# Kernel optimization log

Hardware: AMD Instinct MI355X
Metric: run time of the kernel (lower is better)

## Reference

```python
import jax, jax.numpy as jnp
import numpy as np

B, L, SH, EH, A, T = 128, 200, 512, 512, 512, 3


def setup_inputs() -> dict:
    key = jax.random.key(0)
    ks = jax.random.split(key, 13)
    s = 0.05  # small init scale to keep tanh/sigmoid unsaturated
    return {
        "sent_enc_doc": jax.random.normal(ks[0], (B, L, 2 * SH), jnp.float32),
        "h0_w": jax.random.normal(ks[1], (EH, SH), jnp.float32) * s,
        "h0_b": jax.random.normal(ks[2], (EH,), jnp.float32) * s,
        "gru_w_ih": jax.random.normal(ks[3], (3 * EH, 2 * SH), jnp.float32) * s,
        "gru_w_hh": jax.random.normal(ks[4], (3 * EH, EH), jnp.float32) * s,
        "gru_b_ih": jax.random.normal(ks[5], (3 * EH,), jnp.float32) * s,
        "gru_b_hh": jax.random.normal(ks[6], (3 * EH,), jnp.float32) * s,
        "wq": jax.random.normal(ks[7], (A, EH), jnp.float32) * s,
        "bq": jax.random.normal(ks[8], (A,), jnp.float32) * s,
        "wd": jax.random.normal(ks[9], (A, 2 * SH), jnp.float32) * s,
        "bd": jax.random.normal(ks[10], (A,), jnp.float32) * s,
        "ws": jax.random.normal(ks[11], (1, A), jnp.float32) * s,
        "bs": jax.random.normal(ks[12], (1,), jnp.float32) * s,
    }


def reference(sent_enc_doc, h0_w, h0_b, gru_w_ih, gru_w_hh, gru_b_ih, gru_b_hh,
              wq, bq, wd, bd, ws, bs):
    b, l, d2 = sent_enc_doc.shape
    sh = d2 // 2
    eh = gru_w_hh.shape[1]
    neg = jnp.asarray(-1e6, sent_enc_doc.dtype)

    # h0 = tanh(W * last backward vector), replicated across doc_len
    last_back = sent_enc_doc[:, 0, sh:]                      # (B, SH)
    h0 = jnp.tanh(last_back @ h0_w.T + h0_b)                 # (B, EH)
    h = jnp.broadcast_to(h0[:, None, :], (b, l, eh))         # (B, L, EH)

    s_prev = jnp.zeros((b, l, d2), sent_enc_doc.dtype)
    d_proj = sent_enc_doc @ wd.T + bd                        # (B, L, A) - loop-invariant
    mask = jnp.zeros((b, l), bool)
    rows = jnp.arange(b)

    scores_list, sel_list = [], []
    for _ in range(T):  # fixed, tiny, sequentially-dependent loop
        # GRUCell (torch gate order: r, z, n)
        gx = s_prev @ gru_w_ih.T + gru_b_ih                  # (B, L, 3EH)
        gh = h @ gru_w_hh.T + gru_b_hh                       # (B, L, 3EH)
        xr, xz, xn = jnp.split(gx, 3, axis=-1)
        hr, hz, hn = jnp.split(gh, 3, axis=-1)
        r = jax.nn.sigmoid(xr + hr)
        z = jax.nn.sigmoid(xz + hz)
        n = jnp.tanh(xn + r * hn)
        h = (1.0 - z) * n + z * h                            # (B, L, EH)

        # scorer: ws . tanh(Wq h + Wd s_i)
        score = (jnp.tanh(h @ wq.T + bq + d_proj) @ ws.T + bs)[..., 0]  # (B, L)
        score = jnp.where(mask, neg, score)
        idx = jnp.argmax(score, axis=1)                      # (B,)
        mask = mask.at[rows, idx].set(True)

        # gather the selected sentence encoding, broadcast to all positions
        s_sel = jnp.take_along_axis(sent_enc_doc, idx[:, None, None], axis=1)  # (B,1,2SH)
        s_prev = jnp.broadcast_to(s_sel, (b, l, d2))

        scores_list.append(score)
        sel_list.append(idx)

    sents_scores = jnp.stack(scores_list, axis=1)            # (B, T, L)
    sents_selected = jnp.stack(sel_list, axis=1)             # (B, T)
    return sents_scores, sents_selected
```

## Files before the change

### kernel.cpp

```cpp
#include <hip/hip_runtime.h>
#include <hip/hip_bf16.h>

constexpr int Bn  = 128;
constexpr int Ln  = 200;
constexpr int D2n = 1024;
constexpr int G3n = 1536;
constexpr int Tn  = 3;
constexpr int Nn  = 512;
constexpr int Kn  = 1024;

typedef unsigned short ushort;
typedef float f32x4 __attribute__((ext_vector_type(4)));
typedef __bf16 bf16x8 __attribute__((ext_vector_type(8)));

__device__ __forceinline__ ushort f2bf(float f) {
  unsigned u = __float_as_uint(f);
  unsigned r = (u + 0x7fffu + ((u >> 16) & 1u)) >> 16;
  return (ushort)r;
}
__device__ __forceinline__ float bf2f(ushort h) {
  return __uint_as_float(((unsigned)h) << 16);
}

__device__ __forceinline__ void gld_lds16(const ushort* g, ushort* l) {
  __builtin_amdgcn_global_load_lds(
      (const __attribute__((address_space(1))) unsigned int*)g,
      (__attribute__((address_space(3))) unsigned int*)l, 16, 0, 0);
}

__device__ __forceinline__ float ftanh(float x) {
  float cx = fminf(fmaxf(x, -15.f), 15.f);
  float e  = __expf(2.f * cx);
  return (e - 1.f) * __builtin_amdgcn_rcpf(e + 1.f);
}

__global__ void k_split(const float* __restrict__ W, ushort* __restrict__ hi,
                        ushort* __restrict__ lo) {
  int i = blockIdx.x * 256 + threadIdx.x;
  float4 v = ((const float4*)W)[i];
  ushort4 h, l;
  h.x = f2bf(v.x); l.x = f2bf(v.x - bf2f(h.x));
  h.y = f2bf(v.y); l.y = f2bf(v.y - bf2f(h.y));
  h.z = f2bf(v.z); l.z = f2bf(v.z - bf2f(h.z));
  h.w = f2bf(v.w); l.w = f2bf(v.w - bf2f(h.w));
  ((ushort4*)hi)[i] = h;
  ((ushort4*)lo)[i] = l;
}

__global__ void k_split3(const float* __restrict__ w_ih, const float* __restrict__ w_hh,
                         ushort* __restrict__ WihH, ushort* __restrict__ WihL,
                         ushort* __restrict__ WhhH, ushort* __restrict__ WhhL) {
  int i = blockIdx.x * 256 + threadIdx.x;
  const float* src; ushort* hi; ushort* lo; int off;
  if (i < 393216) { src = w_ih; hi = WihH; lo = WihL; off = i; }
  else            { src = w_hh; hi = WhhH; lo = WhhL; off = i - 393216; }
  float4 v = ((const float4*)src)[off];
  ushort4 h, l;
  h.x = f2bf(v.x); l.x = f2bf(v.x - bf2f(h.x));
  h.y = f2bf(v.y); l.y = f2bf(v.y - bf2f(h.y));
  h.z = f2bf(v.z); l.z = f2bf(v.z - bf2f(h.z));
  h.w = f2bf(v.w); l.w = f2bf(v.w - bf2f(h.w));
  ((ushort4*)hi)[off] = h;
  ((ushort4*)lo)[off] = l;
}

__global__ void k_transp(const float* __restrict__ in, float* __restrict__ out,
                         int R, int C) {
  __shared__ float t[32][33];
  const int x = threadIdx.x, y = threadIdx.y;
  const int c0 = blockIdx.x * 32, r0 = blockIdx.y * 32;
  #pragma unroll
  for (int i = 0; i < 4; ++i)
    t[y + i * 8][x] = in[(size_t)(r0 + y + i * 8) * C + c0 + x];
  __syncthreads();
  #pragma unroll
  for (int i = 0; i < 4; ++i)
    out[(size_t)(c0 + y + i * 8) * R + r0 + x] = t[x][y + i * 8];
}

__launch_bounds__(256)
__global__ void k_h0(const float* __restrict__ sent, const float* __restrict__ W,
                     const float* __restrict__ bias, float* __restrict__ out,
                     ushort* __restrict__ outh, ushort* __restrict__ outl) {
  __shared__ float s[16 * 512];
  const int b0 = blockIdx.y * 16;
  const int jl = threadIdx.x & 63;
  const int j  = blockIdx.x * 64 + jl;
  const int bg = (threadIdx.x >> 6) * 4;

  for (int i = threadIdx.x; i < 2048; i += 256) {
    int r = i >> 7, c = i & 127;
    ((float4*)s)[i] = *(const float4*)(sent + (size_t)(b0 + r) * (Ln * D2n) + 512 + c * 4);
  }
  __syncthreads();

  const float4* w4 = (const float4*)(W + (size_t)j * 512);
  const float4* r0 = (const float4*)(s + (size_t)(bg + 0) * 512);
  const float4* r1 = (const float4*)(s + (size_t)(bg + 1) * 512);
  const float4* r2 = (const float4*)(s + (size_t)(bg + 2) * 512);
  const float4* r3 = (const float4*)(s + (size_t)(bg + 3) * 512);

  float acc0 = 0.f, acc1 = 0.f, acc2 = 0.f, acc3 = 0.f;
  #pragma unroll 4
  for (int k4 = 0; k4 < 128; ++k4) {
    float4 wv = w4[k4];
    float4 a;
    a = r0[k4]; acc0 += wv.x*a.x + wv.y*a.y + wv.z*a.z + wv.w*a.w;
    a = r1[k4]; acc1 += wv.x*a.x + wv.y*a.y + wv.z*a.z + wv.w*a.w;
    a = r2[k4]; acc2 += wv.x*a.x + wv.y*a.y + wv.z*a.z + wv.w*a.w;
    a = r3[k4]; acc3 += wv.x*a.x + wv.y*a.y + wv.z*a.z + wv.w*a.w;
  }
  float bb = bias[j];
  float accs[4] = {acc0, acc1, acc2, acc3};
  #pragma unroll
  for (int i = 0; i < 4; ++i) {
    float v = tanhf(accs[i] + bb);
    size_t o = (size_t)(b0 + bg + i) * 512 + j;
    out[o] = v;
    ushort hv = f2bf(v);
    outh[o] = hv;
    outl[o] = f2bf(v - bf2f(hv));
  }
}

template<int KK>
__device__ __forceinline__ void mfma_tile128(
    const ushort* __restrict__ Ah, const ushort* __restrict__ Al,
    const ushort* __restrict__ Bh, const ushort* __restrict__ Bl,
    const float* __restrict__ bias, float* __restrict__ C, int ldc,
    int m0, int n0) {
  __shared__ __align__(16) ushort sAh[128 * 32];
  __shared__ __align__(16) ushort sAl[128 * 32];
  __shared__ __align__(16) ushort sBh[128 * 32];
  __shared__ __align__(16) ushort sBl[128 * 32];

  const int tid  = threadIdx.x;
  const int wave = tid >> 6, lane = tid & 63;
  const int wy = (wave >> 1) * 64, wx = (wave & 1) * 64;
  const int lm = lane & 15, lq = lane >> 4;
  const int fs = (lq ^ ((lm >> 1) & 3)) * 8;

  const int S0 = (wave * 2 + 0) * 64 + lane;
  const int S1 = (wave * 2 + 1) * 64 + lane;
  const int r0 = S0 >> 2, r1 = S1 >> 2;
  const int c0 = ((S0 & 3) ^ ((r0 >> 1) & 3)) * 8;
  const int c1 = ((S1 & 3) ^ ((r1 >> 1) & 3)) * 8;
  const ushort* pAh0 = Ah + (size_t)(m0 + r0) * KK + c0;
  const ushort* pAh1 = Ah + (size_t)(m0 + r1) * KK + c1;
  const ushort* pAl0 = Al + (size_t)(m0 + r0) * KK + c0;
  const ushort* pAl1 = Al + (size_t)(m0 + r1) * KK + c1;
  const ushort* pBh0 = Bh + (size_t)(n0 + r0) * KK + c0;
  const ushort* pBh1 = Bh + (size_t)(n0 + r1) * KK + c1;
  const ushort* pBl0 = Bl + (size_t)(n0 + r0) * KK + c0;
  const ushort* pBl1 = Bl + (size_t)(n0 + r1) * KK + c1;
  ushort* dA0 = &sAh[S0 * 8]; ushort* dA1 = &sAh[S1 * 8];
  ushort* dL0 = &sAl[S0 * 8]; ushort* dL1 = &sAl[S1 * 8];
  ushort* dB0 = &sBh[S0 * 8]; ushort* dB1 = &sBh[S1 * 8];
  ushort* dC0 = &sBl[S0 * 8]; ushort* dC1 = &sBl[S1 * 8];

  f32x4 acc[4][4] = {};

  for (int ks = 0; ks < KK / 32; ++ks) {
    const int ko = ks * 32;
    gld_lds16(pAh0 + ko, dA0); gld_lds16(pAh1 + ko, dA1);
    gld_lds16(pAl0 + ko, dL0); gld_lds16(pAl1 + ko, dL1);
    gld_lds16(pBh0 + ko, dB0); gld_lds16(pBh1 + ko, dB1);
    gld_lds16(pBl0 + ko, dC0); gld_lds16(pBl1 + ko, dC1);
    __syncthreads();

    bf16x8 ah[4], al[4], bh[4], bl[4];
    #pragma unroll
    for (int mi = 0; mi < 4; ++mi) {
      const int o = (wy + mi * 16 + lm) * 32 + fs;
      ah[mi] = *(const bf16x8*)&sAh[o];
      al[mi] = *(const bf16x8*)&sAl[o];
    }
    #pragma unroll
    for (int ni = 0; ni < 4; ++ni) {
      const int o = (wx + ni * 16 + lm) * 32 + fs;
      bh[ni] = *(const bf16x8*)&sBh[o];
      bl[ni] = *(const bf16x8*)&sBl[o];
    }
    #pragma unroll
    for (int mi = 0; mi < 4; ++mi)
      #pragma unroll
      for (int ni = 0; ni < 4; ++ni) {
        acc[mi][ni] = __builtin_amdgcn_mfma_f32_16x16x32_bf16(ah[mi], bh[ni], acc[mi][ni], 0, 0, 0);
        acc[mi][ni] = __builtin_amdgcn_mfma_f32_16x16x32_bf16(ah[mi], bl[ni], acc[mi][ni], 0, 0, 0);
        acc[mi][ni] = __builtin_amdgcn_mfma_f32_16x16x32_bf16(al[mi], bh[ni], acc[mi][ni], 0, 0, 0);
      }
    __syncthreads();
  }

  #pragma unroll
  for (int ni = 0; ni < 4; ++ni) {
    int col = n0 + wx + ni * 16 + lm;
    float bb = bias[col];
    #pragma unroll
    for (int mi = 0; mi < 4; ++mi) {
      int rbase = m0 + wy + mi * 16 + lq * 4;
      #pragma unroll
      for (int r = 0; r < 4; ++r)
        C[(size_t)(rbase + r) * ldc + col] = acc[mi][ni][r] + bb;
    }
  }
}

__launch_bounds__(256)
__global__ void k_dproj_mfma(const ushort* __restrict__ Ahi, const ushort* __restrict__ Alo,
                             const ushort* __restrict__ Whi, const ushort* __restrict__ Wlo,
                             const float* __restrict__ bias, float* __restrict__ C) {
  const int bid = blockIdx.x;
  mfma_tile128<1024>(Ahi, Alo, Whi, Wlo, bias, C, Nn, (bid % 200) * 128, (bid / 200) * 128);
}

__launch_bounds__(256)
__global__ void k_gates(const ushort* __restrict__ sxh, const ushort* __restrict__ sxl,
                        const float* __restrict__ hOld,
                        const ushort* __restrict__ hh, const ushort* __restrict__ hl,
                        const ushort* __restrict__ WihH, const ushort* __restrict__ WihL,
                        const ushort* __restrict__ WhhH, const ushort* __restrict__ WhhL,
                        const float* __restrict__ b_ih, const float* __restrict__ b_hh,
                        float* __restrict__ hNew, ushort* __restrict__ hhN,
                        ushort* __restrict__ hlN) {
  __shared__ __align__(16) ushort sAh[2][2][64 * 32];
  __shared__ __align__(16) ushort sAl[2][2][64 * 32];
  __shared__ __align__(16) ushort sWh[2][2][48 * 32];
  __shared__ __align__(16) ushort sWl[2][2][48 * 32];

  const int bb  = blockIdx.x >> 5;
  const int j0  = (blockIdx.x & 31) * 16;
  const int rb0 = bb * 64;
  const int tid = threadIdx.x, wave = tid >> 6, lane = tid & 63;
  const int wy = wave * 16;
  const int lm = lane & 15, lq = lane >> 4;
  const int fs = (lq ^ ((lm >> 1) & 3)) * 8;

  const int rA = tid >> 2;
  const int cA = ((tid & 3) ^ ((rA >> 1) & 3)) * 8;
  const bool wOn = tid < 192;
  const int gw = (rA >> 4) * 512 + j0 + (rA & 15);

  const ushort* sxh_r = sxh + (size_t)(rb0 + rA) * 1024 + cA;
  const ushort* sxl_r = sxl + (size_t)(rb0 + rA) * 1024 + cA;
  const ushort* hh_r  = hh  + (size_t)(rb0 + rA) * 512  + cA;
  const ushort* hl_r  = hl  + (size_t)(rb0 + rA) * 512  + cA;
  const ushort* wih_h = WihH + (size_t)gw * 1024 + cA;
  const ushort* wih_l = WihL + (size_t)gw * 1024 + cA;
  const ushort* whh_h = WhhH + (size_t)gw * 512 + cA;
  const ushort* whh_l = WhhL + (size_t)gw * 512 + cA;

  auto stage = [&](int s, int buf) {
    if (s < 16) {
      const int ko = s * 64;
      #pragma unroll
      for (int kk = 0; kk < 2; ++kk) {
        gld_lds16(sxh_r + ko + kk * 32, &sAh[buf][kk][tid * 8]);
        gld_lds16(sxl_r + ko + kk * 32, &sAl[buf][kk][tid * 8]);
        if (wOn) {
          gld_lds16(wih_h + ko + kk * 32, &sWh[buf][kk][tid * 8]);
          gld_lds16(wih_l + ko + kk * 32, &sWl[buf][kk][tid * 8]);
        }
      }
    } else {
      const int ko = (s - 16) * 64;
      #pragma unroll
      for (int kk = 0; kk < 2; ++kk) {
        gld_lds16(hh_r + ko + kk * 32, &sAh[buf][kk][tid * 8]);
        gld_lds16(hl_r + ko + kk * 32, &sAl[buf][kk][tid * 8]);
        if (wOn) {
          gld_lds16(whh_h + ko + kk * 32, &sWh[buf][kk][tid * 8]);
          gld_lds16(whh_l + ko + kk * 32, &sWl[buf][kk][tid * 8]);
        }
      }
    }
  };

  f32x4 ax[3] = {};
  f32x4 ag[3] = {};

  auto compute = [&](int cur, f32x4 (&acc)[3]) {
    const int oA = (wy + lm) * 32 + fs;
    #pragma unroll
    for (int kk = 0; kk < 2; ++kk) {
      bf16x8 fah = *(const bf16x8*)&sAh[cur][kk][oA];
      bf16x8 fal = *(const bf16x8*)&sAl[cur][kk][oA];
      #pragma unroll
      for (int g = 0; g < 3; ++g) {
        const int oW = (g * 16 + lm) * 32 + fs;
        bf16x8 fbh = *(const bf16x8*)&sWh[cur][kk][oW];
        bf16x8 fbl = *(const bf16x8*)&sWl[cur][kk][oW];
        acc[g] = __builtin_amdgcn_mfma_f32_16x16x32_bf16(fah, fbh, acc[g], 0, 0, 0);
        acc[g] = __builtin_amdgcn_mfma_f32_16x16x32_bf16(fah, fbl, acc[g], 0, 0, 0);
        acc[g] = __builtin_amdgcn_mfma_f32_16x16x32_bf16(fal, fbh, acc[g], 0, 0, 0);
      }
    }
  };

  stage(0, 0);
  asm volatile("s_waitcnt vmcnt(0)" ::: "memory");

  for (int s = 0; s < 24; ++s) {
    const int cur = s & 1, nxt = cur ^ 1;
    __syncthreads();
    if (s + 1 < 24) stage(s + 1, nxt);
    if (s < 16) compute(cur, ax); else compute(cur, ag);
    if (s + 1 < 24)
      asm volatile("s_waitcnt vmcnt(0)" ::: "memory");
  }

  const int j = j0 + lm;
  const float bir = b_ih[j], biz = b_ih[512 + j], bin = b_ih[1024 + j];
  const float bhr = b_hh[j], bhz = b_hh[512 + j], bhn = b_hh[1024 + j];
  #pragma unroll
  for (int rr = 0; rr < 4; ++rr) {
    const int b = rb0 + wy + lq * 4 + rr;
    float xr = ax[0][rr] + bir, hr = ag[0][rr] + bhr;
    float xz = ax[1][rr] + biz, hz = ag[1][rr] + bhz;
    float xn = ax[2][rr] + bin, hn = ag[2][rr] + bhn;
    float r = 1.f / (1.f + expf(-(xr + hr)));
    float z = 1.f / (1.f + expf(-(xz + hz)));
    float n = tanhf(xn + r * hn);
    float hv = hOld[(size_t)b * 512 + j];
    float hw = (1.f - z) * n + z * hv;
    hNew[(size_t)b * 512 + j] = hw;
    ushort hbf = f2bf(hw);
    hhN[(size_t)b * 512 + j] = hbf;
    hlN[(size_t)b * 512 + j] = f2bf(hw - bf2f(hbf));
  }
}

__launch_bounds__(256)
__global__ void k_score_argmax(const float* __restrict__ dproj, const float* __restrict__ h,
                               const float* __restrict__ wqT, const float* __restrict__ bq,
                               const float* __restrict__ wsv, const float* __restrict__ bsv,
                               const float* __restrict__ sent,
                               ushort* __restrict__ s_rowh, ushort* __restrict__ s_rowl,
                               int* __restrict__ mask, float* __restrict__ outScores,
                               float* __restrict__ outSel, int t) {
  const int b = blockIdx.x;
  const int tid = threadIdx.x, lane = tid & 63, wv = tid >> 6;
  __shared__ float shb[512];
  __shared__ float sq[512];
  __shared__ float ssc[Ln];
  __shared__ int s_idx;

  if (tid < 128)
    ((float4*)shb)[tid] = ((const float4*)(h + (size_t)b * 512))[tid];
  __syncthreads();

  float qx = 0.f, qy = 0.f;
  #pragma unroll 8
  for (int k = 0; k < 512; ++k) {
    float hk = shb[k];
    float2 w = ((const float2*)(wqT + (size_t)k * 512))[tid];
    qx += hk * w.x; qy += hk * w.y;
  }
  sq[tid * 2]     = qx + bq[tid * 2];
  sq[tid * 2 + 1] = qy + bq[tid * 2 + 1];
  __syncthreads();

  const float4* q4  = (const float4*)sq;
  const float4* ws4 = (const float4*)wsv;
  const float4 qq0 = q4[lane],  qq1 = q4[lane + 64];
  const float4 wv0 = ws4[lane], wv1 = ws4[lane + 64];
  const float bs0 = bsv[0];

  for (int l = wv; l < Ln; l += 4) {
    const float4* dp4 = (const float4*)(dproj + ((size_t)b * Ln + l) * Nn);
    float4 d0 = dp4[lane], d1 = dp4[lane + 64];
    float sum = ftanh(qq0.x + d0.x) * wv0.x + ftanh(qq0.y + d0.y) * wv0.y
              + ftanh(qq0.z + d0.z) * wv0.z + ftanh(qq0.w + d0.w) * wv0.w
              + ftanh(qq1.x + d1.x) * wv1.x + ftanh(qq1.y + d1.y) * wv1.y
              + ftanh(qq1.z + d1.z) * wv1.z + ftanh(qq1.w + d1.w) * wv1.w;
    #pragma unroll
    for (int off = 32; off > 0; off >>= 1) sum += __shfl_xor(sum, off, 64);
    if (lane == 0) {
      float v = sum + bs0;
      if (mask[b * Ln + l]) v = -1000000.0f;
      ssc[l] = v;
      outScores[(size_t)b * (Tn * Ln) + t * Ln + l] = v;
    }
  }
  __syncthreads();

  if (tid < 64) {
    float best = -3.0e38f; int bi = 0;
    for (int l = tid; l < Ln; l += 64) {
      float v = ssc[l];
      if (v > best) { best = v; bi = l; }
    }
    #pragma unroll
    for (int off = 32; off > 0; off >>= 1) {
      float ov = __shfl_down(best, off, 64);
      int   oi = __shfl_down(bi,   off, 64);
      if (ov > best || (ov == best && oi < bi)) { best = ov; bi = oi; }
    }
    if (tid == 0) s_idx = bi;
  }
  __syncthreads();
  int idx = s_idx;
  const float* src = sent + ((size_t)b * Ln + idx) * D2n;
  int k = tid * 4;
  float4 v = *(const float4*)(src + k);
  ushort4 hvec, lvec;
  hvec.x = f2bf(v.x); lvec.x = f2bf(v.x - bf2f(hvec.x));
  hvec.y = f2bf(v.y); lvec.y = f2bf(v.y - bf2f(hvec.y));
  hvec.z = f2bf(v.z); lvec.z = f2bf(v.z - bf2f(hvec.z));
  hvec.w = f2bf(v.w); lvec.w = f2bf(v.w - bf2f(hvec.w));
  *(ushort4*)(s_rowh + (size_t)b * 1024 + k) = hvec;
  *(ushort4*)(s_rowl + (size_t)b * 1024 + k) = lvec;
  if (tid == 0) {
    mask[b * Ln + idx] = 1;
    outSel[(size_t)b * Tn + t] = (float)idx;
  }
}

extern "C" void kernel_launch(void* const* d_in, const int* in_sizes, int n_in,
                              void* d_out, int out_size, void* d_ws, size_t ws_size,
                              hipStream_t stream) {
  const float* sent = (const float*)d_in[0];
  const float* h0_w = (const float*)d_in[1];
  const float* h0_b = (const float*)d_in[2];
  const float* w_ih = (const float*)d_in[3];
  const float* w_hh = (const float*)d_in[4];
  const float* b_ih = (const float*)d_in[5];
  const float* b_hh = (const float*)d_in[6];
  const float* wq   = (const float*)d_in[7];
  const float* bq   = (const float*)d_in[8];
  const float* wd   = (const float*)d_in[9];
  const float* bd   = (const float*)d_in[10];
  const float* wsv  = (const float*)d_in[11];
  const float* bsv  = (const float*)d_in[12];

  float* wsf     = (float*)d_ws;
  float* d_proj  = wsf;
  float* hA      = d_proj + 13107200;
  float* hB      = hA + 65536;
  int*   mask    = (int*)(hB + 65536);
  ushort* Whi    = (ushort*)(mask + 25600);
  ushort* Wlo    = Whi + 524288;
  ushort* hhA    = Wlo + 524288;
  ushort* hlA    = hhA + 65536;
  ushort* hhB    = hlA + 65536;
  ushort* hlB    = hhB + 65536;
  ushort* s_rowh = hlB + 65536;
  ushort* s_rowl = s_rowh + 131072;
  ushort* Ahi    = s_rowl + 131072;
  ushort* Alo    = Ahi + 26214400;

  ushort* WihH   = Ahi;
  ushort* WihL   = WihH + 1572864;
  ushort* WhhH   = WihL + 1572864;
  ushort* WhhL   = WhhH + 786432;
  float*  wqT    = (float*)(WhhL + 786432);

  float* outScores = (float*)d_out;
  float* outSel    = outScores + (size_t)Bn * Tn * Ln;

  hipMemsetAsync(mask, 0, 25600 * sizeof(int), stream);
  hipMemsetAsync(s_rowh, 0, 2 * 131072 * sizeof(ushort), stream);

  k_h0<<<dim3(8, 8), 256, 0, stream>>>(sent, h0_w, h0_b, hA, hhA, hlA);
  k_split<<<512,   256, 0, stream>>>(wd, Whi, Wlo);
  k_split<<<25600, 256, 0, stream>>>(sent, Ahi, Alo);
  k_dproj_mfma<<<800, 256, 0, stream>>>(Ahi, Alo, Whi, Wlo, bd, d_proj);
  k_split3<<<2304, 256, 0, stream>>>(w_ih, w_hh, WihH, WihL, WhhH, WhhL);
  k_transp<<<dim3(16, 16), dim3(32, 8), 0, stream>>>(wq, wqT, 512, 512);

  float* hc = hA;  ushort* hhc = hhA; ushort* hlc = hlA;
  float* hn = hB;  ushort* hhn = hhB; ushort* hln = hlB;
  for (int t = 0; t < Tn; ++t) {
    k_gates<<<64, 256, 0, stream>>>(s_rowh, s_rowl, hc, hhc, hlc,
                                    WihH, WihL, WhhH, WhhL, b_ih, b_hh,
                                    hn, hhn, hln);
    k_score_argmax<<<128, 256, 0, stream>>>(d_proj, hn, wqT, bq, wsv, bsv, sent,
                                            s_rowh, s_rowl, mask,
                                            outScores, outSel, t);
    float* tf = hc; hc = hn; hn = tf;
    ushort* t1 = hhc; hhc = hhn; hhn = t1;
    ushort* t2 = hlc; hlc = hln; hln = t2;
  }
}
```

Measured before the change: 596.6 us.

## Fuse the timestep loop into one cooperative kernel with grid syncs

```diff
diff --git a/kernel.cpp b/kernel.cpp
--- a/kernel.cpp
+++ b/kernel.cpp
@@ -1,5 +1,8 @@
 #include <hip/hip_runtime.h>
 #include <hip/hip_bf16.h>
+#include <hip/hip_cooperative_groups.h>
+
+namespace cg = cooperative_groups;
 
 constexpr int Bn  = 128;
 constexpr int Ln  = 200;
@@ -214,22 +217,17 @@
   mfma_tile128<1024>(Ahi, Alo, Whi, Wlo, bias, C, Nn, (bid % 200) * 128, (bid / 200) * 128);
 }
 
-__launch_bounds__(256)
-__global__ void k_gates(const ushort* __restrict__ sxh, const ushort* __restrict__ sxl,
-                        const float* __restrict__ hOld,
-                        const ushort* __restrict__ hh, const ushort* __restrict__ hl,
-                        const ushort* __restrict__ WihH, const ushort* __restrict__ WihL,
-                        const ushort* __restrict__ WhhH, const ushort* __restrict__ WhhL,
-                        const float* __restrict__ b_ih, const float* __restrict__ b_hh,
-                        float* __restrict__ hNew, ushort* __restrict__ hhN,
-                        ushort* __restrict__ hlN) {
-  __shared__ __align__(16) ushort sAh[2][2][64 * 32];
-  __shared__ __align__(16) ushort sAl[2][2][64 * 32];
-  __shared__ __align__(16) ushort sWh[2][2][48 * 32];
-  __shared__ __align__(16) ushort sWl[2][2][48 * 32];
-
-  const int bb  = blockIdx.x >> 5;
-  const int j0  = (blockIdx.x & 31) * 16;
+__device__ __forceinline__ void gates_work(
+    int wid, ushort* sAh, ushort* sAl, ushort* sWh, ushort* sWl,
+    const ushort* __restrict__ sxh, const ushort* __restrict__ sxl,
+    const float* __restrict__ hOld,
+    const ushort* __restrict__ hh, const ushort* __restrict__ hl,
+    const ushort* __restrict__ WihH, const ushort* __restrict__ WihL,
+    const ushort* __restrict__ WhhH, const ushort* __restrict__ WhhL,
+    const float* __restrict__ b_ih, const float* __restrict__ b_hh,
+    float* __restrict__ hNew, ushort* __restrict__ hhN, ushort* __restrict__ hlN) {
+  const int bb  = wid >> 5;
+  const int j0  = (wid & 31) * 16;
   const int rb0 = bb * 64;
   const int tid = threadIdx.x, wave = tid >> 6, lane = tid & 63;
   const int wy = wave * 16;
@@ -241,72 +239,67 @@
   const bool wOn = tid < 192;
   const int gw = (rA >> 4) * 512 + j0 + (rA & 15);
 
-  const ushort* sxh_r = sxh + (size_t)(rb0 + rA) * 1024 + cA;
-  const ushort* sxl_r = sxl + (size_t)(rb0 + rA) * 1024 + cA;
-  const ushort* hh_r  = hh  + (size_t)(rb0 + rA) * 512  + cA;
-  const ushort* hl_r  = hl  + (size_t)(rb0 + rA) * 512  + cA;
-  const ushort* wih_h = WihH + (size_t)gw * 1024 + cA;
-  const ushort* wih_l = WihL + (size_t)gw * 1024 + cA;
-  const ushort* whh_h = WhhH + (size_t)gw * 512 + cA;
-  const ushort* whh_l = WhhL + (size_t)gw * 512 + cA;
-
-  auto stage = [&](int s, int buf) {
-    if (s < 16) {
-      const int ko = s * 64;
-      #pragma unroll
-      for (int kk = 0; kk < 2; ++kk) {
-        gld_lds16(sxh_r + ko + kk * 32, &sAh[buf][kk][tid * 8]);
-        gld_lds16(sxl_r + ko + kk * 32, &sAl[buf][kk][tid * 8]);
-        if (wOn) {
-          gld_lds16(wih_h + ko + kk * 32, &sWh[buf][kk][tid * 8]);
-          gld_lds16(wih_l + ko + kk * 32, &sWl[buf][kk][tid * 8]);
-        }
-      }
-    } else {
-      const int ko = (s - 16) * 64;
-      #pragma unroll
-      for (int kk = 0; kk < 2; ++kk) {
-        gld_lds16(hh_r + ko + kk * 32, &sAh[buf][kk][tid * 8]);
-        gld_lds16(hl_r + ko + kk * 32, &sAl[buf][kk][tid * 8]);
-        if (wOn) {
-          gld_lds16(whh_h + ko + kk * 32, &sWh[buf][kk][tid * 8]);
-          gld_lds16(whh_l + ko + kk * 32, &sWl[buf][kk][tid * 8]);
-        }
-      }
-    }
-  };
-
   f32x4 ax[3] = {};
   f32x4 ag[3] = {};
 
-  auto compute = [&](int cur, f32x4 (&acc)[3]) {
-    const int oA = (wy + lm) * 32 + fs;
+  for (int ks = 0; ks < 16; ++ks) {
+    const int ko = ks * 64;
     #pragma unroll
     for (int kk = 0; kk < 2; ++kk) {
-      bf16x8 fah = *(const bf16x8*)&sAh[cur][kk][oA];
-      bf16x8 fal = *(const bf16x8*)&sAl[cur][kk][oA];
+      gld_lds16(sxh + (size_t)(rb0 + rA) * 1024 + ko + kk * 32 + cA, &sAh[kk * 2048 + tid * 8]);
+      gld_lds16(sxl + (size_t)(rb0 + rA) * 1024 + ko + kk * 32 + cA, &sAl[kk * 2048 + tid * 8]);
+      if (wOn) {
+        gld_lds16(WihH + (size_t)gw * 1024 + ko + kk * 32 + cA, &sWh[kk * 1536 + tid * 8]);
+        gld_lds16(WihL + (size_t)gw * 1024 + ko + kk * 32 + cA, &sWl[kk * 1536 + tid * 8]);
+      }
+    }
+    __syncthreads();
+    #pragma unroll
+    for (int kk = 0; kk < 2; ++kk) {
+      const int oA = (wy + lm) * 32 + fs;
+      bf16x8 fah = *(const bf16x8*)&sAh[kk * 2048 + oA];
+      bf16x8 fal = *(const bf16x8*)&sAl[kk * 2048 + oA];
       #pragma unroll
       for (int g = 0; g < 3; ++g) {
         const int oW = (g * 16 + lm) * 32 + fs;
-        bf16x8 fbh = *(const bf16x8*)&sWh[cur][kk][oW];
-        bf16x8 fbl = *(const bf16x8*)&sWl[cur][kk][oW];
-        acc[g] = __builtin_amdgcn_mfma_f32_16x16x32_bf16(fah, fbh, acc[g], 0, 0, 0);
-        acc[g] = __builtin_amdgcn_mfma_f32_16x16x32_bf16(fah, fbl, acc[g], 0, 0, 0);
-        acc[g] = __builtin_amdgcn_mfma_f32_16x16x32_bf16(fal, fbh, acc[g], 0, 0, 0);
+        bf16x8 fbh = *(const bf16x8*)&sWh[kk * 1536 + oW];
+        bf16x8 fbl = *(const bf16x8*)&sWl[kk * 1536 + oW];
+        ax[g] = __builtin_amdgcn_mfma_f32_16x16x32_bf16(fah, fbh, ax[g], 0, 0, 0);
+        ax[g] = __builtin_amdgcn_mfma_f32_16x16x32_bf16(fah, fbl, ax[g], 0, 0, 0);
+        ax[g] = __builtin_amdgcn_mfma_f32_16x16x32_bf16(fal, fbh, ax[g], 0, 0, 0);
       }
     }
-  };
-
-  stage(0, 0);
-  asm volatile("s_waitcnt vmcnt(0)" ::: "memory");
-
-  for (int s = 0; s < 24; ++s) {
-    const int cur = s & 1, nxt = cur ^ 1;
     __syncthreads();
-    if (s + 1 < 24) stage(s + 1, nxt);
-    if (s < 16) compute(cur, ax); else compute(cur, ag);
-    if (s + 1 < 24)
-      asm volatile("s_waitcnt vmcnt(0)" ::: "memory");
+  }
+
+  for (int ks = 0; ks < 8; ++ks) {
+    const int ko = ks * 64;
+    #pragma unroll
+    for (int kk = 0; kk < 2; ++kk) {
+      gld_lds16(hh + (size_t)(rb0 + rA) * 512 + ko + kk * 32 + cA, &sAh[kk * 2048 + tid * 8]);
+      gld_lds16(hl + (size_t)(rb0 + rA) * 512 + ko + kk * 32 + cA, &sAl[kk * 2048 + tid * 8]);
+      if (wOn) {
+        gld_lds16(WhhH + (size_t)gw * 512 + ko + kk * 32 + cA, &sWh[kk * 1536 + tid * 8]);
+        gld_lds16(WhhL + (size_t)gw * 512 + ko + kk * 32 + cA, &sWl[kk * 1536 + tid * 8]);
+      }
+    }
+    __syncthreads();
+    #pragma unroll
+    for (int kk = 0; kk < 2; ++kk) {
+      const int oA = (wy + lm) * 32 + fs;
+      bf16x8 fah = *(const bf16x8*)&sAh[kk * 2048 + oA];
+      bf16x8 fal = *(const bf16x8*)&sAl[kk * 2048 + oA];
+      #pragma unroll
+      for (int g = 0; g < 3; ++g) {
+        const int oW = (g * 16 + lm) * 32 + fs;
+        bf16x8 fbh = *(const bf16x8*)&sWh[kk * 1536 + oW];
+        bf16x8 fbl = *(const bf16x8*)&sWl[kk * 1536 + oW];
+        ag[g] = __builtin_amdgcn_mfma_f32_16x16x32_bf16(fah, fbh, ag[g], 0, 0, 0);
+        ag[g] = __builtin_amdgcn_mfma_f32_16x16x32_bf16(fah, fbl, ag[g], 0, 0, 0);
+        ag[g] = __builtin_amdgcn_mfma_f32_16x16x32_bf16(fal, fbh, ag[g], 0, 0, 0);
+      }
+    }
+    __syncthreads();
   }
 
   const int j = j0 + lm;
@@ -330,20 +323,16 @@
   }
 }
 
-__launch_bounds__(256)
-__global__ void k_score_argmax(const float* __restrict__ dproj, const float* __restrict__ h,
-                               const float* __restrict__ wqT, const float* __restrict__ bq,
-                               const float* __restrict__ wsv, const float* __restrict__ bsv,
-                               const float* __restrict__ sent,
-                               ushort* __restrict__ s_rowh, ushort* __restrict__ s_rowl,
-                               int* __restrict__ mask, float* __restrict__ outScores,
-                               float* __restrict__ outSel, int t) {
-  const int b = blockIdx.x;
+__device__ __forceinline__ void score_work(
+    int b, int t, float* shb, float* sq, float* ssc, int* s_idx_p,
+    const float* __restrict__ dproj, const float* __restrict__ h,
+    const float* __restrict__ wqT, const float* __restrict__ bq,
+    const float* __restrict__ wsv, const float* __restrict__ bsv,
+    const float* __restrict__ sent,
+    ushort* __restrict__ s_rowh, ushort* __restrict__ s_rowl,
+    int* __restrict__ mask, float* __restrict__ outScores,
+    float* __restrict__ outSel) {
   const int tid = threadIdx.x, lane = tid & 63, wv = tid >> 6;
-  __shared__ float shb[512];
-  __shared__ float sq[512];
-  __shared__ float ssc[Ln];
-  __shared__ int s_idx;
 
   if (tid < 128)
     ((float4*)shb)[tid] = ((const float4*)(h + (size_t)b * 512))[tid];
@@ -396,10 +385,10 @@
       int   oi = __shfl_down(bi,   off, 64);
       if (ov > best || (ov == best && oi < bi)) { best = ov; bi = oi; }
     }
-    if (tid == 0) s_idx = bi;
+    if (tid == 0) *s_idx_p = bi;
   }
   __syncthreads();
-  int idx = s_idx;
+  int idx = *s_idx_p;
   const float* src = sent + ((size_t)b * Ln + idx) * D2n;
   int k = tid * 4;
   float4 v = *(const float4*)(src + k);
@@ -413,6 +402,49 @@
   if (tid == 0) {
     mask[b * Ln + idx] = 1;
     outSel[(size_t)b * Tn + t] = (float)idx;
+  }
+}
+
+__launch_bounds__(256)
+__global__ void k_tloop(const ushort* __restrict__ WihH, const ushort* __restrict__ WihL,
+                        const ushort* __restrict__ WhhH, const ushort* __restrict__ WhhL,
+                        const float* __restrict__ b_ih, const float* __restrict__ b_hh,
+                        const float* __restrict__ wqT, const float* __restrict__ bq,
+                        const float* __restrict__ wsv, const float* __restrict__ bsv,
+                        const float* __restrict__ dproj, const float* __restrict__ sent,
+                        float* hA, float* hB,
+                        ushort* hhA, ushort* hlA, ushort* hhB, ushort* hlB,
+                        ushort* s_rowh, ushort* s_rowl,
+                        int* mask, float* outScores, float* outSel) {
+  cg::grid_group grid = cg::this_grid();
+  __shared__ __align__(16) ushort sAh[2 * 64 * 32];
+  __shared__ __align__(16) ushort sAl[2 * 64 * 32];
+  __shared__ __align__(16) ushort sWh[2 * 48 * 32];
+  __shared__ __align__(16) ushort sWl[2 * 48 * 32];
+  __shared__ float shb[512];
+  __shared__ float sq[512];
+  __shared__ float ssc[Ln];
+  __shared__ int s_idx;
+
+  float* hc = hA;  float* hn = hB;
+  ushort* hhc = hhA; ushort* hlc = hlA;
+  ushort* hhn = hhB; ushort* hln = hlB;
+
+  for (int t = 0; t < Tn; ++t) {
+    if (blockIdx.x < 64)
+      gates_work(blockIdx.x, sAh, sAl, sWh, sWl,
+                 s_rowh, s_rowl, hc, hhc, hlc,
+                 WihH, WihL, WhhH, WhhL, b_ih, b_hh,
+                 hn, hhn, hln);
+    grid.sync();
+    if (blockIdx.x < 128)
+      score_work(blockIdx.x, t, shb, sq, ssc, &s_idx,
+                 dproj, hn, wqT, bq, wsv, bsv, sent,
+                 s_rowh, s_rowl, mask, outScores, outSel);
+    grid.sync();
+    float* tf = hc; hc = hn; hn = tf;
+    ushort* t1 = hhc; hhc = hhn; hhn = t1;
+    ushort* t2 = hlc; hlc = hln; hln = t2;
   }
 }
 
@@ -468,17 +500,12 @@
   k_split3<<<2304, 256, 0, stream>>>(w_ih, w_hh, WihH, WihL, WhhH, WhhL);
   k_transp<<<dim3(16, 16), dim3(32, 8), 0, stream>>>(wq, wqT, 512, 512);
 
-  float* hc = hA;  ushort* hhc = hhA; ushort* hlc = hlA;
-  float* hn = hB;  ushort* hhn = hhB; ushort* hln = hlB;
-  for (int t = 0; t < Tn; ++t) {
-    k_gates<<<64, 256, 0, stream>>>(s_rowh, s_rowl, hc, hhc, hlc,
-                                    WihH, WihL, WhhH, WhhL, b_ih, b_hh,
-                                    hn, hhn, hln);
-    k_score_argmax<<<128, 256, 0, stream>>>(d_proj, hn, wqT, bq, wsv, bsv, sent,
-                                            s_rowh, s_rowl, mask,
-                                            outScores, outSel, t);
-    float* tf = hc; hc = hn; hn = tf;
-    ushort* t1 = hhc; hhc = hhn; hhn = t1;
-    ushort* t2 = hlc; hlc = hln; hln = t2;
-  }
-}
+  void* args[] = {
+    (void*)&WihH, (void*)&WihL, (void*)&WhhH, (void*)&WhhL,
+    (void*)&b_ih, (void*)&b_hh, (void*)&wqT, (void*)&bq,
+    (void*)&wsv, (void*)&bsv, (void*)&d_proj, (void*)&sent,
+    (void*)&hA, (void*)&hB, (void*)&hhA, (void*)&hlA, (void*)&hhB, (void*)&hlB,
+    (void*)&s_rowh, (void*)&s_rowl, (void*)&mask, (void*)&outScores, (void*)&outSel
+  };
+  hipLaunchCooperativeKernel((void*)k_tloop, dim3(256), dim3(256), args, 0, stream);
+}
```

After: 763.0 us. 27.9% more time.
